# Kernel optimization log

Measured on AMD Instinct MI355X. Metric: run time of the kernel, lower is better.

Reference implementation:

```python
import jax, jax.numpy as jnp
import numpy as np

N_QUBITS = 256
N_LAYERS = 8
BATCH = 65536


def _ln(h, w, b):
    mu = jnp.mean(h, axis=-1, keepdims=True)
    var = jnp.mean((h - mu) ** 2, axis=-1, keepdims=True)
    return (h - mu) * jax.lax.rsqrt(var + 1e-5) * w + b


def setup_inputs() -> dict:
    key = jax.random.key(0)
    ks = jax.random.split(key, 22)
    Q = N_QUBITS
    s = 0.05
    f = jnp.float32
    return {
        "x": jax.random.normal(ks[0], (BATCH, Q), f),
        # type-0 sublayers (layers 0,3,6): Linear(Q,3Q)+LN+GELU+Linear(3Q,Q)
        "dense0_w1": jax.random.normal(ks[1], (3, Q, 3 * Q), f) * s,
        "dense0_b1": jnp.zeros((3, 3 * Q), f),
        "ln_w": jnp.ones((3, 3 * Q), f),
        "ln_b": jnp.zeros((3, 3 * Q), f),
        "dense0_w2": jax.random.normal(ks[2], (3, 3 * Q, Q), f) * s,
        "dense0_b2": jnp.zeros((3, Q), f),
        # type-1 sublayers (layers 1,4,7): Linear(Q,2Q)+SiLU+Linear(2Q,Q)
        "dense1_w1": jax.random.normal(ks[3], (3, Q, 2 * Q), f) * s,
        "dense1_b1": jnp.zeros((3, 2 * Q), f),
        "dense1_w2": jax.random.normal(ks[4], (3, 2 * Q, Q), f) * s,
        "dense1_b2": jnp.zeros((3, Q), f),
        # attention sublayers (layers 2,5): in_proj (qkv) + out_proj, heads=2, seq_len=1
        "attn_wqkv": jax.random.normal(ks[5], (2, Q, 3 * Q), f) * s,
        "attn_bqkv": jnp.zeros((2, 3 * Q), f),
        "attn_wo": jax.random.normal(ks[6], (2, Q, Q), f) * s,
        "attn_bo": jnp.zeros((2, Q), f),
        # per-layer gate params and entanglement matrices (torch randn init)
        "gate_params": jax.random.normal(ks[7], (N_LAYERS, Q, 6), f),
        "ent": jax.random.normal(ks[8], (N_LAYERS, Q, Q), f) * s,
        # nonlinear ops (4 = n_layers//2): Linear+Tanh+Linear
        "nl_w1": jax.random.normal(ks[9], (4, Q, Q), f) * s,
        "nl_b1": jnp.zeros((4, Q), f),
        "nl_w2": jax.random.normal(ks[10], (4, Q, Q), f) * s,
        "nl_b2": jnp.zeros((4, Q), f),
    }


def _forward(x, dense0_w1, dense0_b1, ln_w, ln_b, dense0_w2, dense0_b2,
             dense1_w1, dense1_b1, dense1_w2, dense1_b2,
             attn_wqkv, attn_bqkv, attn_wo, attn_bo,
             gate_params, ent, nl_w1, nl_b1, nl_w2, nl_b2):
    Q = N_QUBITS
    cur = x
    for li in range(N_LAYERS):
        res = cur
        t = li % 3
        if t == 0:
            i = li // 3
            h = cur @ dense0_w1[i] + dense0_b1[i]
            h = _ln(h, ln_w[i], ln_b[i])
            h = jax.nn.gelu(h, approximate=False)  # torch nn.GELU default (erf)
            cur = h @ dense0_w2[i] + dense0_b2[i]
        elif t == 1:
            i = (li - 1) // 3
            h = jax.nn.silu(cur @ dense1_w1[i] + dense1_b1[i])
            cur = h @ dense1_w2[i] + dense1_b2[i]
        else:
            i = (li - 2) // 3
            # seq_len == 1: softmax over a single key is identically 1, so
            # attended == v; q/k projections contribute zero (incl. gradient).
            qkv = cur @ attn_wqkv[i] + attn_bqkv[i]
            v = qkv[:, 2 * Q:]
            cur = v @ attn_wo[i] + attn_bo[i]
        # fused per-qubit gate effects (vectorized over qubits & batch)
        p = gate_params[li]  # [Q, 6]
        lin = jnp.sin(p[:, 0]) + jnp.cos(p[:, 1]) + jnp.tanh(p[:, 2])  # [Q]
        gate = (lin * cur
                + 0.5 * jnp.sin(p[:, 3] * cur + p[:, 4])
                + 0.5 * jnp.cos(p[:, 5] * cur)) / 4.0
        entangled = cur @ jnp.tanh(ent[li])
        cur = (cur + 0.3 * gate + 0.2 * entangled) / 1.5
        if li % 2 == 1:
            j = li // 2  # 0..3, always < 4 here
            nl = jnp.tanh(cur @ nl_w1[j] + nl_b1[j]) @ nl_w2[j] + nl_b2[j]
            cur = cur + 0.1 * nl
        alpha = 0.8 if li < N_LAYERS // 2 else 0.6
        cur = alpha * cur + (1.0 - alpha) * res
        cur = cur / (jnp.linalg.norm(cur, axis=1, keepdims=True) + 1e-8)
        cur = jnp.tanh(cur)
    return cur


def reference(x, dense0_w1, dense0_b1, ln_w, ln_b, dense0_w2, dense0_b2,
              dense1_w1, dense1_b1, dense1_w2, dense1_b2,
              attn_wqkv, attn_bqkv, attn_wo, attn_bo,
              gate_params, ent, nl_w1, nl_b1, nl_w2, nl_b2):
    return _forward(x, dense0_w1, dense0_b1, ln_w, ln_b, dense0_w2, dense0_b2,
                    dense1_w1, dense1_b1, dense1_w2, dense1_b2,
                    attn_wqkv, attn_bqkv, attn_wo, attn_bo,
                    gate_params, ent, nl_w1, nl_b1, nl_w2, nl_b2)
```

## Files before the change

kernel.cpp:

```cpp
#include <hip/hip_runtime.h>
#include <stdint.h>

#define DI __device__ __forceinline__

typedef __bf16 bf16;
typedef __bf16 bf16x8 __attribute__((ext_vector_type(8)));
typedef float  f32x4  __attribute__((ext_vector_type(4)));

constexpr int Q = 256;
constexpr int BATCH = 65536;
constexpr int TM = 64;
constexpr int THREADS = 512;
constexpr int NW = 8;
constexpr int NBLK = BATCH / TM;
constexpr int SC = Q + 8;

constexpr int W0A_OFF = 0;
constexpr int W0B_OFF = W0A_OFF + 3*768*256;
constexpr int W1A_OFF = W0B_OFF + 3*256*768;
constexpr int W1B_OFF = W1A_OFF + 3*512*256;
constexpr int WV_OFF  = W1B_OFF + 3*256*512;
constexpr int WO_OFF  = WV_OFF  + 2*256*256;
constexpr int ENT_OFF = WO_OFF  + 2*256*256;
constexpr int NL1_OFF = ENT_OFF + 8*256*256;
constexpr int NL2_OFF = NL1_OFF + 4*256*256;
constexpr int WEND    = NL2_OFF + 4*256*256;
constexpr size_t F32_BYTE_OFF = (((size_t)WEND*2) + 255) & ~(size_t)255;

constexpr int P_D0B1 = 0;
constexpr int P_LNW  = P_D0B1 + 3*768;
constexpr int P_LNB  = P_LNW  + 3*768;
constexpr int P_D0B2 = P_LNB  + 3*768;
constexpr int P_D1B1 = P_D0B2 + 3*256;
constexpr int P_D1B2 = P_D1B1 + 3*512;
constexpr int P_BQV  = P_D1B2 + 3*256;
constexpr int P_BO   = P_BQV  + 2*256;
constexpr int P_NB1  = P_BO   + 2*256;
constexpr int P_NB2  = P_NB1  + 4*256;
constexpr int P_GLIN = P_NB2  + 4*256;
constexpr int P_GP3  = P_GLIN + 8*256;
constexpr int P_GP4  = P_GP3  + 8*256;
constexpr int P_GP5  = P_GP4  + 8*256;
constexpr int P_END  = P_GP5  + 8*256;
constexpr size_t FLAG_OFF = F32_BYTE_OFF + (size_t)P_END*4;

DI float ldf(const void* p, size_t idx, int f32) {
  return f32 ? ((const float*)p)[idx] : (float)((const bf16*)p)[idx];
}

DI float tanh_fast(float x) {
  float ax = fabsf(x);
  float e  = __expf(-2.0f * ax);
  float r  = (1.0f - e) / (1.0f + e);
  return copysignf(r, x);
}

DI float gelu_f(float x) {
  float ax = fabsf(x) * 0.70710678118654752f;
  float t  = 1.0f / (1.0f + 0.3275911f * ax);
  float y  = t*(0.254829592f + t*(-0.284496736f + t*(1.421413741f +
             t*(-1.453152027f + t*1.061405429f))));
  float er = copysignf(1.0f - y * __expf(-ax*ax), x);
  return 0.5f * x * (1.0f + er);
}

DI f32x4 mfma_bf16(uint4 a, uint4 b, f32x4 c) {
  return __builtin_amdgcn_mfma_f32_16x16x32_bf16(
      __builtin_bit_cast(bf16x8, a), __builtin_bit_cast(bf16x8, b), c, 0, 0, 0);
}

template<int NJ>
DI void zero_acc(f32x4 (&a)[4][NJ]) {
#pragma unroll
  for (int i = 0; i < 4; ++i)
#pragma unroll
    for (int j = 0; j < NJ; ++j) a[i][j] = f32x4{0.f, 0.f, 0.f, 0.f};
}

template<int NJ>
DI void gemm_k256(const bf16* A, const bf16* __restrict__ Bt, int kdb, int koff,
                  f32x4 (&acc)[4][NJ], int wave, int quad, int l16) {
  const bf16* ar[4];
#pragma unroll
  for (int mt = 0; mt < 4; ++mt) ar[mt] = A + (mt*16 + l16)*SC + quad*8;
  const bf16* br[NJ];
#pragma unroll
  for (int nj = 0; nj < NJ; ++nj)
    br[nj] = Bt + (size_t)((nj*NW + wave)*16 + l16)*kdb + koff + quad*8;
#pragma unroll
  for (int ks = 0; ks < 8; ++ks) {
    uint4 av[4];
#pragma unroll
    for (int mt = 0; mt < 4; ++mt) av[mt] = *(const uint4*)(ar[mt] + ks*32);
#pragma unroll
    for (int nj = 0; nj < NJ; ++nj) {
      uint4 bv = *(const uint4*)(br[nj] + ks*32);
#pragma unroll
      for (int mt = 0; mt < 4; ++mt) acc[mt][nj] = mfma_bf16(av[mt], bv, acc[mt][nj]);
    }
  }
}

template<int NJ>
DI void addbias(f32x4 (&a)[4][NJ], const float* __restrict__ b, int wave, int l16) {
#pragma unroll
  for (int nj = 0; nj < NJ; ++nj) {
    float bb = b[(nj*NW + wave)*16 + l16];
#pragma unroll
    for (int mt = 0; mt < 4; ++mt)
#pragma unroll
      for (int reg = 0; reg < 4; ++reg) a[mt][nj][reg] += bb;
  }
}

template<int NJ>
DI void store_t(bf16* dst, const f32x4 (&a)[4][NJ], int wave, int quad, int l16) {
#pragma unroll
  for (int nj = 0; nj < NJ; ++nj) {
    int col = (nj*NW + wave)*16 + l16;
#pragma unroll
    for (int mt = 0; mt < 4; ++mt)
#pragma unroll
      for (int reg = 0; reg < 4; ++reg)
        dst[(mt*16 + quad*4 + reg)*SC + col] = (bf16)a[mt][nj][reg];
  }
}

__global__ void detect_dtype(const uint16_t* __restrict__ xr, int* __restrict__ flag) {
  __shared__ int s_max;
  if (threadIdx.x == 0) s_max = 0;
  __syncthreads();
  int e = 0;
  for (int i = threadIdx.x; i < 4096; i += 256) {
    int ex = (xr[2*i] >> 7) & 0xFF;
    e = e > ex ? e : ex;
  }
  atomicMax(&s_max, e);
  __syncthreads();
  if (threadIdx.x == 0) *flag = (s_max >= 140) ? 1 : 0;
}

__global__ void pack_weights(const void* __restrict__ d0w1, const void* __restrict__ d0w2,
                             const void* __restrict__ d1w1, const void* __restrict__ d1w2,
                             const void* __restrict__ wqkv, const void* __restrict__ wo,
                             const void* __restrict__ ent,  const void* __restrict__ nl1,
                             const void* __restrict__ nl2,  bf16* __restrict__ wsb,
                             const int* __restrict__ flag) {
  const int f32 = *flag;
  int job = blockIdx.y;
  const void* src; int mi, K, N, srcN, col0 = 0, dtanh = 0; long dst;
  if      (job < 3)  { src=d0w1; mi=job;    K=256; N=768; srcN=768; dst=W0A_OFF + (long)mi*768*256; }
  else if (job < 6)  { src=d0w2; mi=job-3;  K=768; N=256; srcN=256; dst=W0B_OFF + (long)mi*256*768; }
  else if (job < 9)  { src=d1w1; mi=job-6;  K=256; N=512; srcN=512; dst=W1A_OFF + (long)mi*512*256; }
  else if (job < 12) { src=d1w2; mi=job-9;  K=512; N=256; srcN=256; dst=W1B_OFF + (long)mi*256*512; }
  else if (job < 14) { src=wqkv; mi=job-12; K=256; N=256; srcN=768; col0=512; dst=WV_OFF + (long)mi*65536; }
  else if (job < 16) { src=wo;   mi=job-14; K=256; N=256; srcN=256; dst=WO_OFF + (long)mi*65536; }
  else if (job < 24) { src=ent;  mi=job-16; K=256; N=256; srcN=256; dst=ENT_OFF + (long)mi*65536; dtanh=1; }
  else if (job < 28) { src=nl1;  mi=job-24; K=256; N=256; srcN=256; dst=NL1_OFF + (long)mi*65536; }
  else               { src=nl2;  mi=job-28; K=256; N=256; srcN=256; dst=NL2_OFF + (long)mi*65536; }
  const size_t base = (size_t)mi * K * srcN;

  int tk = K/64, tn = N/64;
  int tile = blockIdx.x;
  if (tile >= tk*tn) return;
  int ik = tile % tk, in_ = tile / tk;

  __shared__ float t[64][65];
  int tid = threadIdx.x;
  for (int e = tid; e < 4096; e += 256) {
    int r = e >> 6, c = e & 63;
    t[r][c] = ldf(src, base + (size_t)(ik*64 + r)*srcN + col0 + in_*64 + c, f32);
  }
  __syncthreads();
  for (int e = tid; e < 4096; e += 256) {
    int nr = e >> 6, kc = e & 63;
    float v = t[kc][nr];
    if (dtanh) v = tanhf(v);
    wsb[dst + (size_t)(in_*64 + nr)*K + ik*64 + kc] = (bf16)v;
  }
}

__global__ void pack_params(const void* __restrict__ d0b1, const void* __restrict__ lnw,
                            const void* __restrict__ lnb,  const void* __restrict__ d0b2,
                            const void* __restrict__ d1b1, const void* __restrict__ d1b2,
                            const void* __restrict__ bqkv, const void* __restrict__ bo,
                            const void* __restrict__ gp,   const void* __restrict__ nb1,
                            const void* __restrict__ nb2,  float* __restrict__ wsf,
                            const int* __restrict__ flag) {
  const int f32 = *flag;
  int i = blockIdx.x * blockDim.x + threadIdx.x;
  if (i >= P_END) return;
  float v;
  if      (i < P_LNW)  { v = ldf(d0b1, i - P_D0B1, f32); }
  else if (i < P_LNB)  { v = ldf(lnw, i - P_LNW, f32); }
  else if (i < P_D0B2) { v = ldf(lnb, i - P_LNB, f32); }
  else if (i < P_D1B1) { v = ldf(d0b2, i - P_D0B2, f32); }
  else if (i < P_D1B2) { v = ldf(d1b1, i - P_D1B1, f32); }
  else if (i < P_BQV)  { v = ldf(d1b2, i - P_D1B2, f32); }
  else if (i < P_BO)   { int k = i - P_BQV; v = ldf(bqkv, (size_t)(k >> 8)*768 + 512 + (k & 255), f32); }
  else if (i < P_NB1)  { v = ldf(bo, i - P_BO, f32); }
  else if (i < P_NB2)  { v = ldf(nb1, i - P_NB1, f32); }
  else if (i < P_GLIN) { v = ldf(nb2, i - P_NB2, f32); }
  else if (i < P_GP3)  { int k = i - P_GLIN;
                         v = sinf(ldf(gp, (size_t)k*6 + 0, f32)) +
                             cosf(ldf(gp, (size_t)k*6 + 1, f32)) +
                             tanhf(ldf(gp, (size_t)k*6 + 2, f32)); }
  else if (i < P_GP4)  { int k = i - P_GP3; v = ldf(gp, (size_t)k*6 + 3, f32); }
  else if (i < P_GP5)  { int k = i - P_GP4; v = ldf(gp, (size_t)k*6 + 4, f32); }
  else                 { int k = i - P_GP5; v = ldf(gp, (size_t)k*6 + 5, f32); }
  wsf[i] = v;
}

__global__ __launch_bounds__(THREADS, 2)
void vqc_main(const void* __restrict__ x, const bf16* __restrict__ wsb,
              const float* __restrict__ wsf, const int* __restrict__ flag,
              void* __restrict__ out) {
  __shared__ __align__(16) bf16 curT[TM*SC];
  __shared__ __align__(16) bf16 buf0[TM*SC];
  __shared__ float red[2*NW*TM];
  __shared__ float rowa[TM], rowb[TM];

  const int tid  = threadIdx.x;
  const int wave = tid >> 6, lane = tid & 63;
  const int quad = lane >> 4, l16 = lane & 15;
  const size_t rowbase = (size_t)blockIdx.x * TM;
  const int f32io = *flag;

  if (f32io) {
    const float* xf = (const float*)x;
    for (int i = tid; i < TM*Q/4; i += THREADS) {
      int r = i >> 6, c4 = (i & 63) * 4;
      float4 v = *(const float4*)(xf + (rowbase + r)*Q + c4);
      bf16* d = curT + r*SC + c4;
      d[0] = (bf16)v.x; d[1] = (bf16)v.y; d[2] = (bf16)v.z; d[3] = (bf16)v.w;
    }
  } else {
    const bf16* xb = (const bf16*)x;
    for (int i = tid; i < TM*Q/8; i += THREADS) {
      int r = i >> 5, c8 = (i & 31) * 8;
      *(uint4*)(curT + r*SC + c8) = *(const uint4*)(xb + (rowbase + r)*Q + c8);
    }
  }
  __syncthreads();

#pragma unroll 1
  for (int li = 0; li < 8; ++li) {
    const int t = li % 3;
    f32x4 acc2[4][2]; zero_acc<2>(acc2);

    if (t == 0) {
      const int i = li / 3;
      f32x4 acc[4][6]; zero_acc<6>(acc);
      gemm_k256<6>(curT, wsb + W0A_OFF + (size_t)i*768*256, 256, 0, acc, wave, quad, l16);
      const float* b1 = wsf + P_D0B1 + i*768;
#pragma unroll
      for (int nj = 0; nj < 6; ++nj) {
        float bb = b1[(nj*NW + wave)*16 + l16];
#pragma unroll
        for (int mt = 0; mt < 4; ++mt)
#pragma unroll
          for (int reg = 0; reg < 4; ++reg) acc[mt][nj][reg] += bb;
      }
#pragma unroll
      for (int mt = 0; mt < 4; ++mt) {
#pragma unroll
        for (int reg = 0; reg < 4; ++reg) {
          float sa = 0.f, sb = 0.f;
#pragma unroll
          for (int nj = 0; nj < 6; ++nj) { float v = acc[mt][nj][reg]; sa += v; sb += v*v; }
#pragma unroll
          for (int m = 1; m < 16; m <<= 1) { sa += __shfl_xor(sa, m, 64); sb += __shfl_xor(sb, m, 64); }
          if (l16 == 0) {
            int row = mt*16 + quad*4 + reg;
            red[wave*TM + row] = sa; red[NW*TM + wave*TM + row] = sb;
          }
        }
      }
      __syncthreads();
      if (tid < TM) {
        float sa = 0.f, sb = 0.f;
#pragma unroll
        for (int w = 0; w < NW; ++w) { sa += red[w*TM + tid]; sb += red[NW*TM + w*TM + tid]; }
        float mu  = sa * (1.0f/768.0f);
        float var = sb * (1.0f/768.0f) - mu*mu;
        rowa[tid] = mu; rowb[tid] = rsqrtf(fmaxf(var, 0.f) + 1e-5f);
      }
      __syncthreads();
      const float* lw = wsf + P_LNW + i*768;
      const float* lb = wsf + P_LNB + i*768;
#pragma unroll
      for (int nj = 0; nj < 6; ++nj) {
        int col = (nj*NW + wave)*16 + l16;
        float w_ = lw[col], bb = lb[col];
#pragma unroll
        for (int mt = 0; mt < 4; ++mt)
#pragma unroll
          for (int reg = 0; reg < 4; ++reg) {
            int row = mt*16 + quad*4 + reg;
            acc[mt][nj][reg] = gelu_f((acc[mt][nj][reg] - rowa[row]) * rowb[row] * w_ + bb);
          }
      }
      const bf16* w2 = wsb + W0B_OFF + (size_t)i*256*768;
#pragma unroll 1
      for (int c = 0; c < 3; ++c) {
#pragma unroll
        for (int njl = 0; njl < 2; ++njl) {
          int nj = 2*c + njl;
          int col = (njl*NW + wave)*16 + l16;
#pragma unroll
          for (int mt = 0; mt < 4; ++mt)
#pragma unroll
            for (int reg = 0; reg < 4; ++reg)
              buf0[(mt*16 + quad*4 + reg)*SC + col] = (bf16)acc[mt][nj][reg];
        }
        __syncthreads();
        gemm_k256<2>(buf0, w2, 768, 256*c, acc2, wave, quad, l16);
        __syncthreads();
      }
      addbias<2>(acc2, wsf + P_D0B2 + i*256, wave, l16);
    } else if (t == 1) {
      const int i = (li - 1) / 3;
      f32x4 acc[4][4]; zero_acc<4>(acc);
      gemm_k256<4>(curT, wsb + W1A_OFF + (size_t)i*512*256, 256, 0, acc, wave, quad, l16);
      const float* b1 = wsf + P_D1B1 + i*512;
#pragma unroll
      for (int nj = 0; nj < 4; ++nj) {
        float bb = b1[(nj*NW + wave)*16 + l16];
#pragma unroll
        for (int mt = 0; mt < 4; ++mt)
#pragma unroll
          for (int reg = 0; reg < 4; ++reg) {
            float xv = acc[mt][nj][reg] + bb;
            acc[mt][nj][reg] = xv / (1.0f + __expf(-xv));
          }
      }
      const bf16* w2 = wsb + W1B_OFF + (size_t)i*256*512;
#pragma unroll 1
      for (int c = 0; c < 2; ++c) {
#pragma unroll
        for (int njl = 0; njl < 2; ++njl) {
          int nj = 2*c + njl;
          int col = (njl*NW + wave)*16 + l16;
#pragma unroll
          for (int mt = 0; mt < 4; ++mt)
#pragma unroll
            for (int reg = 0; reg < 4; ++reg)
              buf0[(mt*16 + quad*4 + reg)*SC + col] = (bf16)acc[mt][nj][reg];
        }
        __syncthreads();
        gemm_k256<2>(buf0, w2, 512, 256*c, acc2, wave, quad, l16);
        __syncthreads();
      }
      addbias<2>(acc2, wsf + P_D1B2 + i*256, wave, l16);
    } else {
      const int i = (li - 2) / 3;
      f32x4 acc[4][2]; zero_acc<2>(acc);
      gemm_k256<2>(curT, wsb + WV_OFF + (size_t)i*65536, 256, 0, acc, wave, quad, l16);
      addbias<2>(acc, wsf + P_BQV + i*256, wave, l16);
      store_t<2>(buf0, acc, wave, quad, l16);
      __syncthreads();
      gemm_k256<2>(buf0, wsb + WO_OFF + (size_t)i*65536, 256, 0, acc2, wave, quad, l16);
      addbias<2>(acc2, wsf + P_BO + i*256, wave, l16);
      __syncthreads();
    }

    store_t<2>(buf0, acc2, wave, quad, l16);
    __syncthreads();
    f32x4 acc3[4][2]; zero_acc<2>(acc3);
    gemm_k256<2>(buf0, wsb + ENT_OFF + (size_t)li*65536, 256, 0, acc3, wave, quad, l16);
    __syncthreads();

    const float* gl = wsf + P_GLIN + li*256;
    const float* g3 = wsf + P_GP3  + li*256;
    const float* g4 = wsf + P_GP4  + li*256;
    const float* g5 = wsf + P_GP5  + li*256;
#pragma unroll
    for (int nj = 0; nj < 2; ++nj) {
      int col = (nj*NW + wave)*16 + l16;
      float lin = gl[col], p3 = g3[col], p4 = g4[col], p5 = g5[col];
#pragma unroll
      for (int mt = 0; mt < 4; ++mt)
#pragma unroll
        for (int reg = 0; reg < 4; ++reg) {
          float v = acc2[mt][nj][reg];
          float gate = (lin*v + 0.5f*__sinf(p3*v + p4) + 0.5f*__cosf(p5*v)) * 0.25f;
          acc2[mt][nj][reg] = (v + 0.3f*gate + 0.2f*acc3[mt][nj][reg]) * (1.0f/1.5f);
        }
    }

    if (li & 1) {
      const int j = li >> 1;
      store_t<2>(buf0, acc2, wave, quad, l16);
      __syncthreads();
      f32x4 a4[4][2]; zero_acc<2>(a4);
      gemm_k256<2>(buf0, wsb + NL1_OFF + (size_t)j*65536, 256, 0, a4, wave, quad, l16);
      const float* nb1p = wsf + P_NB1 + j*256;
      __syncthreads();
#pragma unroll
      for (int nj = 0; nj < 2; ++nj) {
        int col = (nj*NW + wave)*16 + l16;
        float bb = nb1p[col];
#pragma unroll
        for (int mt = 0; mt < 4; ++mt)
#pragma unroll
          for (int reg = 0; reg < 4; ++reg)
            buf0[(mt*16 + quad*4 + reg)*SC + col] = (bf16)tanh_fast(a4[mt][nj][reg] + bb);
      }
      __syncthreads();
      f32x4 a5[4][2]; zero_acc<2>(a5);
      gemm_k256<2>(buf0, wsb + NL2_OFF + (size_t)j*65536, 256, 0, a5, wave, quad, l16);
      const float* nb2p = wsf + P_NB2 + j*256;
#pragma unroll
      for (int nj = 0; nj < 2; ++nj) {
        float bb = nb2p[(nj*NW + wave)*16 + l16];
#pragma unroll
        for (int mt = 0; mt < 4; ++mt)
#pragma unroll
          for (int reg = 0; reg < 4; ++reg) acc2[mt][nj][reg] += 0.1f*(a5[mt][nj][reg] + bb);
      }
    }

    const float alpha = (li < 4) ? 0.8f : 0.6f;
    const float beta  = 1.0f - alpha;
#pragma unroll
    for (int nj = 0; nj < 2; ++nj) {
      int col = (nj*NW + wave)*16 + l16;
#pragma unroll
      for (int mt = 0; mt < 4; ++mt)
#pragma unroll
        for (int reg = 0; reg < 4; ++reg) {
          int row = mt*16 + quad*4 + reg;
          acc2[mt][nj][reg] = alpha*acc2[mt][nj][reg] + beta*(float)curT[row*SC + col];
        }
    }
#pragma unroll
    for (int mt = 0; mt < 4; ++mt) {
#pragma unroll
      for (int reg = 0; reg < 4; ++reg) {
        float s = 0.f;
#pragma unroll
        for (int nj = 0; nj < 2; ++nj) s += acc2[mt][nj][reg]*acc2[mt][nj][reg];
#pragma unroll
        for (int m = 1; m < 16; m <<= 1) s += __shfl_xor(s, m, 64);
        if (l16 == 0) red[wave*TM + mt*16 + quad*4 + reg] = s;
      }
    }
    __syncthreads();
    if (tid < TM) {
      float s = 0.f;
#pragma unroll
      for (int w = 0; w < NW; ++w) s += red[w*TM + tid];
      rowa[tid] = 1.0f / (sqrtf(fmaxf(s, 0.f)) + 1e-8f);
    }
    __syncthreads();
#pragma unroll
    for (int nj = 0; nj < 2; ++nj) {
      int col = (nj*NW + wave)*16 + l16;
#pragma unroll
      for (int mt = 0; mt < 4; ++mt)
#pragma unroll
        for (int reg = 0; reg < 4; ++reg) {
          int row = mt*16 + quad*4 + reg;
          curT[row*SC + col] = (bf16)tanh_fast(acc2[mt][nj][reg] * rowa[row]);
        }
    }
    __syncthreads();
  }

  if (f32io) {
    float* of = (float*)out;
    for (int i = tid; i < TM*Q/4; i += THREADS) {
      int r = i >> 6, c4 = (i & 63) * 4;
      const bf16* s = curT + r*SC + c4;
      float4 v = make_float4((float)s[0], (float)s[1], (float)s[2], (float)s[3]);
      *(float4*)(of + (rowbase + r)*Q + c4) = v;
    }
  } else {
    bf16* ob = (bf16*)out;
    for (int i = tid; i < TM*Q/8; i += THREADS) {
      int r = i >> 5, c8 = (i & 31) * 8;
      *(uint4*)(ob + (rowbase + r)*Q + c8) = *(const uint4*)(curT + r*SC + c8);
    }
  }
}

extern "C" void kernel_launch(void* const* d_in, const int* in_sizes, int n_in,
                              void* d_out, int out_size, void* d_ws, size_t ws_size,
                              hipStream_t stream) {
  const void* x    = d_in[0];
  const void* d0w1 = d_in[1];
  const void* d0b1 = d_in[2];
  const void* lnw  = d_in[3];
  const void* lnb  = d_in[4];
  const void* d0w2 = d_in[5];
  const void* d0b2 = d_in[6];
  const void* d1w1 = d_in[7];
  const void* d1b1 = d_in[8];
  const void* d1w2 = d_in[9];
  const void* d1b2 = d_in[10];
  const void* wqkv = d_in[11];
  const void* bqkv = d_in[12];
  const void* wo   = d_in[13];
  const void* bo   = d_in[14];
  const void* gp   = d_in[15];
  const void* ent  = d_in[16];
  const void* nl1  = d_in[17];
  const void* nb1  = d_in[18];
  const void* nl2  = d_in[19];
  const void* nb2  = d_in[20];

  bf16*  wsb  = (bf16*)d_ws;
  float* wsf  = (float*)((char*)d_ws + F32_BYTE_OFF);
  int*   flag = (int*)((char*)d_ws + FLAG_OFF);

  detect_dtype<<<dim3(1), dim3(256), 0, stream>>>((const uint16_t*)x, flag);
  pack_weights<<<dim3(48, 32), dim3(256), 0, stream>>>(
      d0w1, d0w2, d1w1, d1w2, wqkv, wo, ent, nl1, nl2, wsb, flag);
  pack_params<<<dim3((P_END + 255)/256), dim3(256), 0, stream>>>(
      d0b1, lnw, lnb, d0b2, d1b1, d1b2, bqkv, bo, gp, nb1, nb2, wsf, flag);
  vqc_main<<<dim3(NBLK), dim3(THREADS), 0, stream>>>(x, wsb, wsf, flag, d_out);
}
```

Measured before the change: 1.673 ms.

## Chunk first-layer GEMMs to cut accumulator registers, recompute for LayerNorm pass

The dense sublayers now compute the hidden activation in 256-column chunks instead of holding the full 768 or 512 wide accumulator tile in registers. For the LayerNorm sublayer, a first pass over the chunks gathers row sums and sums of squares, and a second pass recomputes each chunk's GEMM to apply normalisation and GELU before feeding the second GEMM. The SiLU sublayer is chunked and fused directly with no recompute. This is meant to reduce register pressure so occupancy can rise or spills disappear, at the cost of doing the first LayerNorm-sublayer GEMM twice. A reversed-k variant is used in the stats pass so the summation order differs.

```diff
diff --git a/kernel.cpp b/kernel.cpp
--- a/kernel.cpp
+++ b/kernel.cpp
@@ -89,6 +89,30 @@
     br[nj] = Bt + (size_t)((nj*NW + wave)*16 + l16)*kdb + koff + quad*8;
 #pragma unroll
   for (int ks = 0; ks < 8; ++ks) {
+    uint4 av[4];
+#pragma unroll
+    for (int mt = 0; mt < 4; ++mt) av[mt] = *(const uint4*)(ar[mt] + ks*32);
+#pragma unroll
+    for (int nj = 0; nj < NJ; ++nj) {
+      uint4 bv = *(const uint4*)(br[nj] + ks*32);
+#pragma unroll
+      for (int mt = 0; mt < 4; ++mt) acc[mt][nj] = mfma_bf16(av[mt], bv, acc[mt][nj]);
+    }
+  }
+}
+
+template<int NJ>
+DI void gemm_k256r(const bf16* A, const bf16* __restrict__ Bt, int kdb, int koff,
+                   f32x4 (&acc)[4][NJ], int wave, int quad, int l16) {
+  const bf16* ar[4];
+#pragma unroll
+  for (int mt = 0; mt < 4; ++mt) ar[mt] = A + (mt*16 + l16)*SC + quad*8;
+  const bf16* br[NJ];
+#pragma unroll
+  for (int nj = 0; nj < NJ; ++nj)
+    br[nj] = Bt + (size_t)((nj*NW + wave)*16 + l16)*kdb + koff + quad*8;
+#pragma unroll
+  for (int ks = 7; ks >= 0; --ks) {
     uint4 av[4];
 #pragma unroll
     for (int mt = 0; mt < 4; ++mt) av[mt] = *(const uint4*)(ar[mt] + ks*32);
@@ -250,24 +274,36 @@
 
     if (t == 0) {
       const int i = li / 3;
-      f32x4 acc[4][6]; zero_acc<6>(acc);
-      gemm_k256<6>(curT, wsb + W0A_OFF + (size_t)i*768*256, 256, 0, acc, wave, quad, l16);
+      const bf16* w1 = wsb + W0A_OFF + (size_t)i*768*256;
+      const bf16* w2 = wsb + W0B_OFF + (size_t)i*256*768;
       const float* b1 = wsf + P_D0B1 + i*768;
-#pragma unroll
-      for (int nj = 0; nj < 6; ++nj) {
-        float bb = b1[(nj*NW + wave)*16 + l16];
-#pragma unroll
-        for (int mt = 0; mt < 4; ++mt)
-#pragma unroll
-          for (int reg = 0; reg < 4; ++reg) acc[mt][nj][reg] += bb;
+
+      float sa4[4][4], sb4[4][4];
+#pragma unroll
+      for (int mt = 0; mt < 4; ++mt)
+#pragma unroll
+        for (int reg = 0; reg < 4; ++reg) { sa4[mt][reg] = 0.f; sb4[mt][reg] = 0.f; }
+#pragma unroll 1
+      for (int c = 0; c < 3; ++c) {
+        f32x4 acs[4][2]; zero_acc<2>(acs);
+        gemm_k256r<2>(curT, w1 + (size_t)c*256*256, 256, 0, acs, wave, quad, l16);
+#pragma unroll
+        for (int njl = 0; njl < 2; ++njl) {
+          float bb = b1[c*256 + (njl*NW + wave)*16 + l16];
+#pragma unroll
+          for (int mt = 0; mt < 4; ++mt)
+#pragma unroll
+            for (int reg = 0; reg < 4; ++reg) {
+              float v = acs[mt][njl][reg] + bb;
+              sa4[mt][reg] += v; sb4[mt][reg] += v*v;
+            }
+        }
       }
 #pragma unroll
       for (int mt = 0; mt < 4; ++mt) {
 #pragma unroll
         for (int reg = 0; reg < 4; ++reg) {
-          float sa = 0.f, sb = 0.f;
-#pragma unroll
-          for (int nj = 0; nj < 6; ++nj) { float v = acc[mt][nj][reg]; sa += v; sb += v*v; }
+          float sa = sa4[mt][reg], sb = sb4[mt][reg];
 #pragma unroll
           for (int m = 1; m < 16; m <<= 1) { sa += __shfl_xor(sa, m, 64); sb += __shfl_xor(sb, m, 64); }
           if (l16 == 0) {
@@ -286,32 +322,26 @@
         rowa[tid] = mu; rowb[tid] = rsqrtf(fmaxf(var, 0.f) + 1e-5f);
       }
       __syncthreads();
-      const float* lw = wsf + P_LNW + i*768;
-      const float* lb = wsf + P_LNB + i*768;
-#pragma unroll
-      for (int nj = 0; nj < 6; ++nj) {
-        int col = (nj*NW + wave)*16 + l16;
-        float w_ = lw[col], bb = lb[col];
-#pragma unroll
-        for (int mt = 0; mt < 4; ++mt)
-#pragma unroll
-          for (int reg = 0; reg < 4; ++reg) {
-            int row = mt*16 + quad*4 + reg;
-            acc[mt][nj][reg] = gelu_f((acc[mt][nj][reg] - rowa[row]) * rowb[row] * w_ + bb);
-          }
-      }
-      const bf16* w2 = wsb + W0B_OFF + (size_t)i*256*768;
+
 #pragma unroll 1
       for (int c = 0; c < 3; ++c) {
+        f32x4 acs[4][2]; zero_acc<2>(acs);
+        gemm_k256<2>(curT, w1 + (size_t)c*256*256, 256, 0, acs, wave, quad, l16);
+        const float* lw = wsf + P_LNW + i*768 + c*256;
+        const float* lb = wsf + P_LNB + i*768 + c*256;
 #pragma unroll
         for (int njl = 0; njl < 2; ++njl) {
-          int nj = 2*c + njl;
           int col = (njl*NW + wave)*16 + l16;
+          float bb = b1[c*256 + col];
+          float w_ = lw[col], lbb = lb[col];
 #pragma unroll
           for (int mt = 0; mt < 4; ++mt)
 #pragma unroll
-            for (int reg = 0; reg < 4; ++reg)
-              buf0[(mt*16 + quad*4 + reg)*SC + col] = (bf16)acc[mt][nj][reg];
+            for (int reg = 0; reg < 4; ++reg) {
+              int row = mt*16 + quad*4 + reg;
+              float h = gelu_f((acs[mt][njl][reg] + bb - rowa[row]) * rowb[row] * w_ + lbb);
+              buf0[row*SC + col] = (bf16)h;
+            }
         }
         __syncthreads();
         gemm_k256<2>(buf0, w2, 768, 256*c, acc2, wave, quad, l16);
@@ -320,32 +350,24 @@
       addbias<2>(acc2, wsf + P_D0B2 + i*256, wave, l16);
     } else if (t == 1) {
       const int i = (li - 1) / 3;
-      f32x4 acc[4][4]; zero_acc<4>(acc);
-      gemm_k256<4>(curT, wsb + W1A_OFF + (size_t)i*512*256, 256, 0, acc, wave, quad, l16);
+      const bf16* w1 = wsb + W1A_OFF + (size_t)i*512*256;
+      const bf16* w2 = wsb + W1B_OFF + (size_t)i*256*512;
       const float* b1 = wsf + P_D1B1 + i*512;
-#pragma unroll
-      for (int nj = 0; nj < 4; ++nj) {
-        float bb = b1[(nj*NW + wave)*16 + l16];
-#pragma unroll
-        for (int mt = 0; mt < 4; ++mt)
-#pragma unroll
-          for (int reg = 0; reg < 4; ++reg) {
-            float xv = acc[mt][nj][reg] + bb;
-            acc[mt][nj][reg] = xv / (1.0f + __expf(-xv));
-          }
-      }
-      const bf16* w2 = wsb + W1B_OFF + (size_t)i*256*512;
 #pragma unroll 1
       for (int c = 0; c < 2; ++c) {
+        f32x4 acs[4][2]; zero_acc<2>(acs);
+        gemm_k256<2>(curT, w1 + (size_t)c*256*256, 256, 0, acs, wave, quad, l16);
 #pragma unroll
         for (int njl = 0; njl < 2; ++njl) {
-          int nj = 2*c + njl;
           int col = (njl*NW + wave)*16 + l16;
+          float bb = b1[c*256 + col];
 #pragma unroll
           for (int mt = 0; mt < 4; ++mt)
 #pragma unroll
-            for (int reg = 0; reg < 4; ++reg)
-              buf0[(mt*16 + quad*4 + reg)*SC + col] = (bf16)acc[mt][nj][reg];
+            for (int reg = 0; reg < 4; ++reg) {
+              float xv = acs[mt][njl][reg] + bb;
+              buf0[(mt*16 + quad*4 + reg)*SC + col] = (bf16)(xv / (1.0f + __expf(-xv)));
+            }
         }
         __syncthreads();
         gemm_k256<2>(buf0, w2, 512, 256*c, acc2, wave, quad, l16);
```

Result: no change. 1.701 ms (+1.7%).
